# Kernel optimization log

Measured on AMD Instinct MI355X. Metric: run time of the kernel, lower is better.

Reference implementation:

```python
import jax, jax.numpy as jnp
import numpy as np

B = 64      # graphs per batch
N = 1024    # nodes per graph (equal-size graphs -> static top-k)
D = 256     # in_dim
DEG = 16    # avg degree
K = 512     # k = ratio * N, ratio = 0.5
E = B * N * DEG
NT = B * N


def setup_inputs() -> dict:
    key = jax.random.key(0)
    ks = jax.random.split(key, 8)
    feature = jax.random.normal(ks[0], (NT, D), jnp.float32)
    gid = jnp.repeat(jnp.arange(B), N * DEG)          # graph id per edge
    src = gid * N + jax.random.randint(ks[1], (E,), 0, N)
    dst = gid * N + jax.random.randint(ks[2], (E,), 0, N)
    label = jax.random.randint(ks[3], (B,), 0, 2)
    W = jax.random.normal(ks[4], (D, 1), jnp.float32) / np.sqrt(D)   # GraphConv weight
    b = jnp.zeros((1,), jnp.float32)                                  # GraphConv bias
    lin1_w = jax.random.normal(ks[5], (2, 1), jnp.float32) / np.sqrt(2.0)
    lin1_b = jnp.zeros((1,), jnp.float32)
    return dict(feature=feature, src=src, dst=dst, label=label,
                W=W, b=b, lin1_w=lin1_w, lin1_b=lin1_b)


def reference(feature, src, dst, label, W, b, lin1_w, lin1_b):
    fdt = feature.dtype
    # ---- get_bias_score: distance-to-class-center score ----
    node_label = jnp.repeat(label, N).astype(fdt)                 # [NT]
    gemb = feature.reshape(B, N, D).mean(axis=1)                  # AvgPooling per graph [B, D]
    lab_f = label.astype(fdt)                                     # [B]
    n1 = jnp.maximum(lab_f.sum(), 1.0)
    n0 = jnp.maximum((1.0 - lab_f).sum(), 1.0)
    center0 = (gemb * (1.0 - lab_f)[:, None]).sum(0) / n0         # [D]
    center1 = (gemb * lab_f[:, None]).sum(0) / n1                 # [D]
    d0 = jnp.sqrt(((feature - center0) ** 2).sum(-1))             # [NT]
    d1 = jnp.sqrt(((feature - center1) ** 2).sum(-1))             # [NT]
    score_distance = (d0 - d1) * ((node_label - 0.5) * 2.0)       # [NT]
    # ---- GraphConv(in_dim, 1), norm='both' (DGL semantics) ----
    ones_e = jnp.ones((E,), fdt)
    deg_out = jax.ops.segment_sum(ones_e, src, NT)
    deg_in = jax.ops.segment_sum(ones_e, dst, NT)
    ns = jnp.maximum(deg_out, 1.0) ** -0.5                        # src-side norm
    nd = jnp.maximum(deg_in, 1.0) ** -0.5                         # dst-side norm
    h = (feature @ W) * ns[:, None]                               # project first (out<in) [NT,1]
    agg = jax.ops.segment_sum(h[src], dst, NT)                    # [NT,1]
    score_gcn = (agg * nd[:, None] + b)[:, 0]                     # [NT]
    # ---- combine two scores with lin1: Linear(2, 1) ----
    score = jnp.stack([score_gcn, score_distance], axis=-1) @ lin1_w + lin1_b  # [NT,1]
    sflat = score[:, 0]
    # ---- per-graph top-k (mytopk with equal-size graphs -> static k) ----
    _, idx = jax.lax.top_k(sflat.reshape(B, N), K)                # [B,K] local indices
    perm = (idx + (jnp.arange(B) * N)[:, None]).reshape(-1)       # [B*K] global indices
    mask = jnp.ones((NT,), bool).at[perm].set(False)
    perm_com = jnp.nonzero(mask, size=NT - B * K)[0]              # complement, static size
    # ---- gather + tanh-gated features ----
    feature_dis = feature[perm] * jnp.tanh(sflat[perm])[:, None]          # [B*K, D]
    feature_com = feature[perm_com] * jnp.tanh(sflat[perm_com])[:, None]  # [B*(N-K), D]
    score_soft = jax.nn.softmax(score, axis=0)                    # softmax over all nodes
    return feature_dis, feature_com, perm, perm_com, score_soft
```

## Files before the change

kernel.cpp:

```cpp
#include <hip/hip_runtime.h>
#include <math.h>

#define Bg   64
#define Nn   1024
#define Dd   256
#define EPG  16384
#define NT   (Bg * Nn)
#define Kk   512

#define OFF_DIS   0
#define OFF_COM   8388608
#define OFF_PERM  16777216
#define OFF_PCOM  16809984
#define OFF_SOFT  16842752

#define WS_H0     0
#define WS_SFLAT  (NT * 4)
#define WS_GPART  (NT * 4 * 2)
#define WS_REDM   (WS_GPART + 512 * 256 * 4)
#define WS_REDS   (WS_REDM + 256)
#define WS_C0     (WS_REDS + 256)
#define WS_C1     (WS_C0 + 1024)
#define WS_PERMI  (WS_C1 + 1024)
#define WS_PCOMI  (WS_PERMI + 32768 * 4)
#define WS_SGCN   (WS_PCOMI + 32768 * 4)

__global__ __launch_bounds__(256) void k_col(
        const float* __restrict__ f, const float* __restrict__ W,
        float* __restrict__ gpart, float* __restrict__ h0) {
    __shared__ float scol[1024];
    int blk = blockIdx.x, t = threadIdx.x;
    int base = blk * 128;
    int lane = t & 63, wid = t >> 6;
    const float4* f4 = (const float4*)f;
    const float4* W4 = (const float4*)W;
    float4 w = W4[lane];
    float4 cs = make_float4(0.f, 0.f, 0.f, 0.f);
    for (int r = 0; r < 32; ++r) {
        int row = base + wid * 32 + r;
        float4 v = f4[(size_t)row * 64 + lane];
        cs.x += v.x; cs.y += v.y; cs.z += v.z; cs.w += v.w;
        float d = v.x * w.x + v.y * w.y + v.z * w.z + v.w * w.w;
        for (int o = 32; o > 0; o >>= 1) d += __shfl_xor(d, o);
        if (lane == 0) h0[row] = d;
    }
    ((float4*)scol)[wid * 64 + lane] = cs;
    __syncthreads();
    gpart[blk * Dd + t] = scol[t] + scol[Dd + t] + scol[2 * Dd + t] + scol[3 * Dd + t];
}

__global__ __launch_bounds__(1024) void k_edge(
        const int* __restrict__ src, const int* __restrict__ dst,
        const int* __restrict__ label, const float* __restrict__ h0,
        const float* __restrict__ gpart, const float* __restrict__ b,
        float* __restrict__ sgcn, float* __restrict__ c0, float* __restrict__ c1) {
    __shared__ uint4 ep4[4096];
    __shared__ int   sdo[1024];
    __shared__ int   sdi[1024];
    __shared__ float shn[1024];
    __shared__ float ssc[1024];
    __shared__ float sc0[1024];
    __shared__ float sc1[1024];

    int g = blockIdx.x, t = threadIdx.x;
    sdo[t] = 0; sdi[t] = 0;

    if (g == 0) {
        int col = t & 255, chunk = t >> 8;
        float a0 = 0.f, a1 = 0.f;
        for (int gg = chunk * 16; gg < chunk * 16 + 16; ++gg) {
            float v = 0.f;
            #pragma unroll
            for (int p = 0; p < 8; ++p) v += gpart[(gg * 8 + p) * Dd + col];
            if (label[gg]) a1 += v; else a0 += v;
        }
        sc0[t] = a0; sc1[t] = a1;
        __syncthreads();
        if (t < Dd) {
            int n1 = 0;
            for (int gg = 0; gg < Bg; ++gg) n1 += label[gg];
            float fn1 = fmaxf((float)n1, 1.f);
            float fn0 = fmaxf((float)(Bg - n1), 1.f);
            float s0 = sc0[t] + sc0[256 + t] + sc0[512 + t] + sc0[768 + t];
            float s1 = sc1[t] + sc1[256 + t] + sc1[512 + t] + sc1[768 + t];
            c0[t] = s0 * (1.f / (float)Nn) / fn0;
            c1[t] = s1 * (1.f / (float)Nn) / fn1;
        }
    }
    __syncthreads();

    {
        const int4* s4 = (const int4*)(src + g * EPG);
        const int4* d4 = (const int4*)(dst + g * EPG);
        #pragma unroll
        for (int i = t; i < EPG / 4; i += 1024) {
            int4 ss = s4[i];
            int4 dd = d4[i];
            int s0 = ss.x & (Nn - 1), s1 = ss.y & (Nn - 1), s2 = ss.z & (Nn - 1), s3 = ss.w & (Nn - 1);
            int e0 = dd.x & (Nn - 1), e1 = dd.y & (Nn - 1), e2 = dd.z & (Nn - 1), e3 = dd.w & (Nn - 1);
            uint4 pk;
            pk.x = (unsigned)(s0 | (e0 << 16));
            pk.y = (unsigned)(s1 | (e1 << 16));
            pk.z = (unsigned)(s2 | (e2 << 16));
            pk.w = (unsigned)(s3 | (e3 << 16));
            ep4[i] = pk;
            atomicAdd(&sdo[s0], 1); atomicAdd(&sdo[s1], 1);
            atomicAdd(&sdo[s2], 1); atomicAdd(&sdo[s3], 1);
            atomicAdd(&sdi[e0], 1); atomicAdd(&sdi[e1], 1);
            atomicAdd(&sdi[e2], 1); atomicAdd(&sdi[e3], 1);
        }
    }
    __syncthreads();

    {
        int dg = sdo[t]; if (dg < 1) dg = 1;
        shn[t] = h0[g * Nn + t] / sqrtf((float)dg);
        ssc[t] = 0.f;
    }
    __syncthreads();

    #pragma unroll
    for (int i = t; i < EPG / 4; i += 1024) {
        uint4 pk = ep4[i];
        atomicAdd(&ssc[pk.x >> 16], shn[pk.x & 0xFFFF]);
        atomicAdd(&ssc[pk.y >> 16], shn[pk.y & 0xFFFF]);
        atomicAdd(&ssc[pk.z >> 16], shn[pk.z & 0xFFFF]);
        atomicAdd(&ssc[pk.w >> 16], shn[pk.w & 0xFFFF]);
    }
    __syncthreads();

    {
        int dg = sdi[t]; if (dg < 1) dg = 1;
        sgcn[g * Nn + t] = ssc[t] / sqrtf((float)dg) + b[0];
    }
}

__global__ __launch_bounds__(256) void k_score(
        const float* __restrict__ f, const float* __restrict__ c0,
        const float* __restrict__ c1, const float* __restrict__ sgcn,
        const int* __restrict__ label, const float* __restrict__ lw,
        const float* __restrict__ lb, float* __restrict__ sflat) {
    int t = threadIdx.x;
    int grp = t >> 4, sub = t & 15;
    int row = blockIdx.x * 16 + grp;
    int g = row >> 10;
    const float4* f4 = (const float4*)f;
    float4 c0r[4], c1r[4];
    #pragma unroll
    for (int it = 0; it < 4; ++it) {
        c0r[it] = ((const float4*)c0)[it * 16 + sub];
        c1r[it] = ((const float4*)c1)[it * 16 + sub];
    }
    float a0 = 0.f, a1 = 0.f;
    size_t bofs = (size_t)row * 64;
    #pragma unroll
    for (int it = 0; it < 4; ++it) {
        float4 v = f4[bofs + it * 16 + sub];
        float dx;
        dx = v.x - c0r[it].x; a0 += dx * dx;
        dx = v.y - c0r[it].y; a0 += dx * dx;
        dx = v.z - c0r[it].z; a0 += dx * dx;
        dx = v.w - c0r[it].w; a0 += dx * dx;
        dx = v.x - c1r[it].x; a1 += dx * dx;
        dx = v.y - c1r[it].y; a1 += dx * dx;
        dx = v.z - c1r[it].z; a1 += dx * dx;
        dx = v.w - c1r[it].w; a1 += dx * dx;
    }
    #pragma unroll
    for (int o = 1; o < 16; o <<= 1) {
        a0 += __shfl_xor(a0, o);
        a1 += __shfl_xor(a1, o);
    }
    if (sub == 0) {
        float sgn = label[g] ? 1.f : -1.f;
        float sdist = (sqrtf(a0) - sqrtf(a1)) * sgn;
        sflat[row] = sgcn[row] * lw[0] + sdist * lw[1] + lb[0];
    }
}

__global__ __launch_bounds__(512) void k_topk(
        const float* __restrict__ sflat, int* __restrict__ permI,
        int* __restrict__ pcomI, float* __restrict__ out,
        float* __restrict__ redM, float* __restrict__ redS) {
    __shared__ unsigned long long sk[1024];
    __shared__ int   sflag[1024];
    __shared__ int   swave[8];
    __shared__ float sred[16];
    int g = blockIdx.x, t = threadIdx.x;
    int lane = t & 63, w = t >> 6;
    float v0 = sflat[g * Nn + t];
    float v1 = sflat[g * Nn + t + 512];
    unsigned u0 = __float_as_uint(v0);
    unsigned u1 = __float_as_uint(v1);
    unsigned o0 = u0 ^ ((u0 >> 31) ? 0xFFFFFFFFu : 0x80000000u);
    unsigned o1 = u1 ^ ((u1 >> 31) ? 0xFFFFFFFFu : 0x80000000u);
    sk[t]       = ((unsigned long long)o0 << 32) | (unsigned)(1023 - t);
    sk[t + 512] = ((unsigned long long)o1 << 32) | (unsigned)(1023 - (t + 512));
    __syncthreads();
    for (int k = 2; k <= 1024; k <<= 1) {
        for (int j = k >> 1; j > 0; j >>= 1) {
            int l = ((t & ~(j - 1)) << 1) | (t & (j - 1));
            int r = l | j;
            unsigned long long a = sk[l], bk = sk[r];
            bool up = ((l & k) == 0);
            if ((a < bk) == up) { sk[l] = bk; sk[r] = a; }
            __syncthreads();
        }
    }
    sflag[t] = 1; sflag[t + 512] = 1;
    __syncthreads();
    {
        int loc = 1023 - (int)(sk[t] & 0xFFFFFFFFu);
        sflag[loc] = 0;
        int gi = g * Nn + loc;
        permI[g * Kk + t] = gi;
        out[OFF_PERM + g * Kk + t] = (float)gi;
    }
    __syncthreads();
    int f0 = sflag[2 * t], f1 = sflag[2 * t + 1];
    int f2 = f0 + f1;
    int inc = f2;
    for (int o = 1; o < 64; o <<= 1) {
        int y = __shfl_up(inc, o);
        if (lane >= o) inc += y;
    }
    if (lane == 63) swave[w] = inc;
    __syncthreads();
    if (t < 8) {
        int a = swave[t];
        for (int o = 1; o < 8; o <<= 1) {
            int y = __shfl_up(a, o);
            if (t >= o) a += y;
        }
        swave[t] = a;
    }
    __syncthreads();
    int basep = ((w > 0) ? swave[w - 1] : 0) + (inc - f2);
    if (f0) {
        int gi = g * Nn + 2 * t;
        pcomI[g * Kk + basep] = gi;
        out[OFF_PCOM + g * Kk + basep] = (float)gi;
    }
    if (f1) {
        int pos = basep + f0;
        int gi = g * Nn + 2 * t + 1;
        pcomI[g * Kk + pos] = gi;
        out[OFF_PCOM + g * Kk + pos] = (float)gi;
    }
    float m = fmaxf(v0, v1);
    for (int o = 32; o > 0; o >>= 1) m = fmaxf(m, __shfl_xor(m, o));
    if (lane == 0) sred[w] = m;
    __syncthreads();
    if (t < 8) {
        float a = sred[t];
        for (int o = 4; o > 0; o >>= 1) a = fmaxf(a, __shfl_xor(a, o));
        if (t == 0) sred[0] = a;
    }
    __syncthreads();
    m = sred[0];
    float s = expf(v0 - m) + expf(v1 - m);
    for (int o = 32; o > 0; o >>= 1) s += __shfl_xor(s, o);
    if (lane == 0) sred[8 + w] = s;
    __syncthreads();
    if (t < 8) {
        float a = sred[8 + t];
        for (int o = 4; o > 0; o >>= 1) a += __shfl_xor(a, o);
        if (t == 0) { redM[g] = m; redS[g] = a; }
    }
}

__global__ void k_write(const float* __restrict__ f, const int* __restrict__ permI,
                        const int* __restrict__ pcomI, const float* __restrict__ sflat,
                        const float* __restrict__ redM, const float* __restrict__ redS,
                        float* __restrict__ out) {
    __shared__ float sMS[2];
    int t = threadIdx.x;
    if (t < 64) {
        float m = redM[t];
        float mm = m;
        for (int o = 32; o > 0; o >>= 1) mm = fmaxf(mm, __shfl_xor(mm, o));
        float s = redS[t] * expf(m - mm);
        for (int o = 32; o > 0; o >>= 1) s += __shfl_xor(s, o);
        if (t == 0) { sMS[0] = mm; sMS[1] = s; }
    }
    __syncthreads();
    float M = sMS[0], S = sMS[1];
    if (t < 4) {
        int i = blockIdx.x * 4 + t;
        out[OFF_SOFT + i] = expf(sflat[i] - M) / S;
    }
    int j = blockIdx.x * 4 + (t >> 6);
    int lane = t & 63;
    int row = (j < 32768) ? permI[j] : pcomI[j - 32768];
    float tv = tanhf(sflat[row]);
    const float4* f4 = (const float4*)f;
    float4* o4 = (float4*)out;
    float4 v = f4[(size_t)row * 64 + lane];
    o4[(size_t)j * 64 + lane] = make_float4(v.x * tv, v.y * tv, v.z * tv, v.w * tv);
}

extern "C" void kernel_launch(void* const* d_in, const int* in_sizes, int n_in,
                              void* d_out, int out_size, void* d_ws, size_t ws_size,
                              hipStream_t stream) {
    const float* feature = (const float*)d_in[0];
    const int*   src     = (const int*)d_in[1];
    const int*   dst     = (const int*)d_in[2];
    const int*   label   = (const int*)d_in[3];
    const float* W       = (const float*)d_in[4];
    const float* b       = (const float*)d_in[5];
    const float* lw      = (const float*)d_in[6];
    const float* lb      = (const float*)d_in[7];
    float* out = (float*)d_out;
    char*  ws  = (char*)d_ws;

    float* h0    = (float*)(ws + WS_H0);
    float* sflat = (float*)(ws + WS_SFLAT);
    float* gpart = (float*)(ws + WS_GPART);
    float* redM  = (float*)(ws + WS_REDM);
    float* redS  = (float*)(ws + WS_REDS);
    float* c0    = (float*)(ws + WS_C0);
    float* c1    = (float*)(ws + WS_C1);
    int*   permI = (int*)(ws + WS_PERMI);
    int*   pcomI = (int*)(ws + WS_PCOMI);
    float* sgcn  = (float*)(ws + WS_SGCN);

    k_col  <<<512,     256,  0, stream>>>(feature, W, gpart, h0);
    k_edge <<<Bg,      1024, 0, stream>>>(src, dst, label, h0, gpart, b, sgcn, c0, c1);
    k_score<<<NT / 16, 256,  0, stream>>>(feature, c0, c1, sgcn, label, lw, lb, sflat);
    k_topk <<<Bg,      512,  0, stream>>>(sflat, permI, pcomI, out, redM, redS);
    k_write<<<NT / 4,  256,  0, stream>>>(feature, permI, pcomI, sflat, redM, redS, out);
}
```

Baseline: 211.5 us.

## Batch multiple rows per thread group in col, score and write kernels

Restructures three bandwidth-bound kernels so each thread group issues several independent row loads before computing. k_col moves from one wavefront per 32 sequential rows to 16-lane groups handling 4 rows each over 1024 blocks, with gpart doubled in size and k_edge reading 16 partials per graph. k_score processes 2 rows per group and k_write 4 rows per wave. The aim is more memory-level parallelism and fewer serialized shuffle reductions, at the cost of higher register use per thread.

```diff
diff --git a/kernel.cpp b/kernel.cpp
--- a/kernel.cpp
+++ b/kernel.cpp
@@ -17,7 +17,7 @@
 #define WS_H0     0
 #define WS_SFLAT  (NT * 4)
 #define WS_GPART  (NT * 4 * 2)
-#define WS_REDM   (WS_GPART + 512 * 256 * 4)
+#define WS_REDM   (WS_GPART + 1024 * 256 * 4)
 #define WS_REDS   (WS_REDM + 256)
 #define WS_C0     (WS_REDS + 256)
 #define WS_C1     (WS_C0 + 1024)
@@ -28,25 +28,51 @@
 __global__ __launch_bounds__(256) void k_col(
         const float* __restrict__ f, const float* __restrict__ W,
         float* __restrict__ gpart, float* __restrict__ h0) {
-    __shared__ float scol[1024];
+    __shared__ float4 scol4[1024];
     int blk = blockIdx.x, t = threadIdx.x;
-    int base = blk * 128;
-    int lane = t & 63, wid = t >> 6;
+    int gid = t >> 4, sub = t & 15;
+    int base = blk * 64 + gid * 4;
     const float4* f4 = (const float4*)f;
     const float4* W4 = (const float4*)W;
-    float4 w = W4[lane];
-    float4 cs = make_float4(0.f, 0.f, 0.f, 0.f);
-    for (int r = 0; r < 32; ++r) {
-        int row = base + wid * 32 + r;
-        float4 v = f4[(size_t)row * 64 + lane];
-        cs.x += v.x; cs.y += v.y; cs.z += v.z; cs.w += v.w;
-        float d = v.x * w.x + v.y * w.y + v.z * w.z + v.w * w.w;
-        for (int o = 32; o > 0; o >>= 1) d += __shfl_xor(d, o);
-        if (lane == 0) h0[row] = d;
-    }
-    ((float4*)scol)[wid * 64 + lane] = cs;
-    __syncthreads();
-    gpart[blk * Dd + t] = scol[t] + scol[Dd + t] + scol[2 * Dd + t] + scol[3 * Dd + t];
+    float4 w[4];
+    #pragma unroll
+    for (int it = 0; it < 4; ++it) w[it] = W4[it * 16 + sub];
+    float4 cs[4];
+    #pragma unroll
+    for (int it = 0; it < 4; ++it) cs[it] = make_float4(0.f, 0.f, 0.f, 0.f);
+    float4 v[4][4];
+    #pragma unroll
+    for (int k = 0; k < 4; ++k) {
+        size_t bofs = (size_t)(base + k) * 64;
+        #pragma unroll
+        for (int it = 0; it < 4; ++it) v[k][it] = f4[bofs + it * 16 + sub];
+    }
+    #pragma unroll
+    for (int k = 0; k < 4; ++k) {
+        float d = 0.f;
+        #pragma unroll
+        for (int it = 0; it < 4; ++it) {
+            cs[it].x += v[k][it].x; cs[it].y += v[k][it].y;
+            cs[it].z += v[k][it].z; cs[it].w += v[k][it].w;
+            d += v[k][it].x * w[it].x + v[k][it].y * w[it].y
+               + v[k][it].z * w[it].z + v[k][it].w * w[it].w;
+        }
+        #pragma unroll
+        for (int o = 1; o < 16; o <<= 1) d += __shfl_xor(d, o);
+        if (sub == 0) h0[base + k] = d;
+    }
+    #pragma unroll
+    for (int it = 0; it < 4; ++it) scol4[gid * 64 + it * 16 + sub] = cs[it];
+    __syncthreads();
+    if (t < 64) {
+        float4 s = make_float4(0.f, 0.f, 0.f, 0.f);
+        #pragma unroll
+        for (int g2 = 0; g2 < 16; ++g2) {
+            float4 u = scol4[g2 * 64 + t];
+            s.x += u.x; s.y += u.y; s.z += u.z; s.w += u.w;
+        }
+        ((float4*)(gpart + blk * Dd))[t] = s;
+    }
 }
 
 __global__ __launch_bounds__(1024) void k_edge(
@@ -71,7 +97,7 @@
         for (int gg = chunk * 16; gg < chunk * 16 + 16; ++gg) {
             float v = 0.f;
             #pragma unroll
-            for (int p = 0; p < 8; ++p) v += gpart[(gg * 8 + p) * Dd + col];
+            for (int p = 0; p < 16; ++p) v += gpart[(gg * 16 + p) * Dd + col];
             if (label[gg]) a1 += v; else a0 += v;
         }
         sc0[t] = a0; sc1[t] = a1;
@@ -141,9 +167,9 @@
         const int* __restrict__ label, const float* __restrict__ lw,
         const float* __restrict__ lb, float* __restrict__ sflat) {
     int t = threadIdx.x;
-    int grp = t >> 4, sub = t & 15;
-    int row = blockIdx.x * 16 + grp;
-    int g = row >> 10;
+    int gid = t >> 4, sub = t & 15;
+    int row0 = blockIdx.x * 32 + gid * 2;
+    int g = row0 >> 10;
     const float4* f4 = (const float4*)f;
     float4 c0r[4], c1r[4];
     #pragma unroll
@@ -151,30 +177,40 @@
         c0r[it] = ((const float4*)c0)[it * 16 + sub];
         c1r[it] = ((const float4*)c1)[it * 16 + sub];
     }
-    float a0 = 0.f, a1 = 0.f;
-    size_t bofs = (size_t)row * 64;
-    #pragma unroll
-    for (int it = 0; it < 4; ++it) {
-        float4 v = f4[bofs + it * 16 + sub];
-        float dx;
-        dx = v.x - c0r[it].x; a0 += dx * dx;
-        dx = v.y - c0r[it].y; a0 += dx * dx;
-        dx = v.z - c0r[it].z; a0 += dx * dx;
-        dx = v.w - c0r[it].w; a0 += dx * dx;
-        dx = v.x - c1r[it].x; a1 += dx * dx;
-        dx = v.y - c1r[it].y; a1 += dx * dx;
-        dx = v.z - c1r[it].z; a1 += dx * dx;
-        dx = v.w - c1r[it].w; a1 += dx * dx;
-    }
-    #pragma unroll
-    for (int o = 1; o < 16; o <<= 1) {
-        a0 += __shfl_xor(a0, o);
-        a1 += __shfl_xor(a1, o);
-    }
-    if (sub == 0) {
-        float sgn = label[g] ? 1.f : -1.f;
-        float sdist = (sqrtf(a0) - sqrtf(a1)) * sgn;
-        sflat[row] = sgcn[row] * lw[0] + sdist * lw[1] + lb[0];
+    float sgn = label[g] ? 1.f : -1.f;
+    float lw0 = lw[0], lw1 = lw[1], lb0 = lb[0];
+    float4 v[2][4];
+    #pragma unroll
+    for (int r = 0; r < 2; ++r) {
+        size_t bofs = (size_t)(row0 + r) * 64;
+        #pragma unroll
+        for (int it = 0; it < 4; ++it) v[r][it] = f4[bofs + it * 16 + sub];
+    }
+    #pragma unroll
+    for (int r = 0; r < 2; ++r) {
+        float a0 = 0.f, a1 = 0.f;
+        #pragma unroll
+        for (int it = 0; it < 4; ++it) {
+            float dx;
+            dx = v[r][it].x - c0r[it].x; a0 += dx * dx;
+            dx = v[r][it].y - c0r[it].y; a0 += dx * dx;
+            dx = v[r][it].z - c0r[it].z; a0 += dx * dx;
+            dx = v[r][it].w - c0r[it].w; a0 += dx * dx;
+            dx = v[r][it].x - c1r[it].x; a1 += dx * dx;
+            dx = v[r][it].y - c1r[it].y; a1 += dx * dx;
+            dx = v[r][it].z - c1r[it].z; a1 += dx * dx;
+            dx = v[r][it].w - c1r[it].w; a1 += dx * dx;
+        }
+        #pragma unroll
+        for (int o = 1; o < 16; o <<= 1) {
+            a0 += __shfl_xor(a0, o);
+            a1 += __shfl_xor(a1, o);
+        }
+        if (sub == 0) {
+            int row = row0 + r;
+            float sdist = (sqrtf(a0) - sqrtf(a1)) * sgn;
+            sflat[row] = sgcn[row] * lw0 + sdist * lw1 + lb0;
+        }
     }
 }
 
@@ -269,10 +305,11 @@
     }
 }
 
-__global__ void k_write(const float* __restrict__ f, const int* __restrict__ permI,
-                        const int* __restrict__ pcomI, const float* __restrict__ sflat,
-                        const float* __restrict__ redM, const float* __restrict__ redS,
-                        float* __restrict__ out) {
+__global__ __launch_bounds__(256) void k_write(
+        const float* __restrict__ f, const int* __restrict__ permI,
+        const int* __restrict__ pcomI, const float* __restrict__ sflat,
+        const float* __restrict__ redM, const float* __restrict__ redS,
+        float* __restrict__ out) {
     __shared__ float sMS[2];
     int t = threadIdx.x;
     if (t < 64) {
@@ -285,18 +322,29 @@
     }
     __syncthreads();
     float M = sMS[0], S = sMS[1];
-    if (t < 4) {
-        int i = blockIdx.x * 4 + t;
+    if (t < 16) {
+        int i = blockIdx.x * 16 + t;
         out[OFF_SOFT + i] = expf(sflat[i] - M) / S;
     }
-    int j = blockIdx.x * 4 + (t >> 6);
-    int lane = t & 63;
-    int row = (j < 32768) ? permI[j] : pcomI[j - 32768];
-    float tv = tanhf(sflat[row]);
+    int w = t >> 6, lane = t & 63;
+    int j0 = blockIdx.x * 16 + w * 4;
+    int rows[4];
+    float tv[4];
+    #pragma unroll
+    for (int i = 0; i < 4; ++i) {
+        int j = j0 + i;
+        rows[i] = (j < 32768) ? permI[j] : pcomI[j - 32768];
+    }
+    #pragma unroll
+    for (int i = 0; i < 4; ++i) tv[i] = tanhf(sflat[rows[i]]);
     const float4* f4 = (const float4*)f;
     float4* o4 = (float4*)out;
-    float4 v = f4[(size_t)row * 64 + lane];
-    o4[(size_t)j * 64 + lane] = make_float4(v.x * tv, v.y * tv, v.z * tv, v.w * tv);
+    #pragma unroll
+    for (int i = 0; i < 4; ++i) {
+        float4 v = f4[(size_t)rows[i] * 64 + lane];
+        o4[(size_t)(j0 + i) * 64 + lane] =
+            make_float4(v.x * tv[i], v.y * tv[i], v.z * tv[i], v.w * tv[i]);
+    }
 }
 
 extern "C" void kernel_launch(void* const* d_in, const int* in_sizes, int n_in,
@@ -324,9 +372,9 @@
     int*   pcomI = (int*)(ws + WS_PCOMI);
     float* sgcn  = (float*)(ws + WS_SGCN);
 
-    k_col  <<<512,     256,  0, stream>>>(feature, W, gpart, h0);
-    k_edge <<<Bg,      1024, 0, stream>>>(src, dst, label, h0, gpart, b, sgcn, c0, c1);
-    k_score<<<NT / 16, 256,  0, stream>>>(feature, c0, c1, sgcn, label, lw, lb, sflat);
-    k_topk <<<Bg,      512,  0, stream>>>(sflat, permI, pcomI, out, redM, redS);
-    k_write<<<NT / 4,  256,  0, stream>>>(feature, permI, pcomI, sflat, redM, redS, out);
-}
+    k_col  <<<1024, 256,  0, stream>>>(feature, W, gpart, h0);
+    k_edge <<<Bg,   1024, 0, stream>>>(src, dst, label, h0, gpart, b, sgcn, c0, c1);
+    k_score<<<2048, 256,  0, stream>>>(feature, c0, c1, sgcn, label, lw, lb, sflat);
+    k_topk <<<Bg,   512,  0, stream>>>(sflat, permI, pcomI, out, redM, redS);
+    k_write<<<4096, 256,  0, stream>>>(feature, permI, pcomI, sflat, redM, redS, out);
+}
```

New measurement: 201.9 us. 1.05x faster.
